# Kernel optimization log

Hardware: AMD Instinct MI355X
Metric: run time of the kernel (lower is better)

Reference implementation:

```python
import jax, jax.numpy as jnp
import numpy as np

T, B, D, H, L = 1024, 64, 512, 512, 2


def setup_inputs() -> dict:
    key = jax.random.key(0)
    ks = jax.random.split(key, 10)
    s = 1.0 / np.sqrt(D)
    return {
        "x": jax.random.normal(ks[0], (T, B, D), jnp.float32),
        "hidden": jax.random.normal(ks[1], (L, B, H), jnp.float32),
        "fc_w": jax.random.normal(ks[2], (D, D), jnp.float32) * s,
        "fc_b": jax.random.normal(ks[3], (D,), jnp.float32) * s,
        "w0": jax.random.normal(ks[4], (H, D), jnp.float32) * s,
        "b0": jax.random.normal(ks[5], (H,), jnp.float32) * s,
        "u0": jax.random.uniform(ks[6], (H,), jnp.float32, -1.0, 1.0),
        "w1": jax.random.normal(ks[7], (H, H), jnp.float32) * s,
        "b1": jax.random.normal(ks[8], (H,), jnp.float32) * s,
        "u1": jax.random.uniform(ks[9], (H,), jnp.float32, -1.0, 1.0),
    }


def _indrnn_layer(inp, h0, w, b, u):
    # Precompute input projection for all timesteps: [T, B, H]
    pre = jnp.einsum("tbd,hd->tbh", inp, w) + b

    def step(h, p):
        h_new = jax.nn.relu(p + u * h)  # elementwise recurrent weight
        return h_new, h_new

    h_last, outs = jax.lax.scan(step, h0, pre)
    return outs, h_last


def reference(x, hidden, fc_w, fc_b, w0, b0, u0, w1, b1, u1):
    # fc layer before the IndRNN stack
    x = jnp.einsum("tbd,ed->tbe", x, fc_w) + fc_b
    out0, h0 = _indrnn_layer(x, hidden[0], w0, b0, u0)
    out1, h1 = _indrnn_layer(out0, hidden[1], w1, b1, u1)
    hn = jnp.stack([h0, h1], axis=0)  # [L, B, H]
    return out1, hn
```

## Files before the change

### kernel.cpp

```cpp
#include <hip/hip_runtime.h>
#include <hip/hip_bf16.h>
#include <cstdint>
#include <cstddef>

#define T_DIM 1024
#define B_DIM 64
#define D_DIM 512
#define H_DIM 512
#define TBROWS (T_DIM * B_DIM)
#define BH (B_DIM * H_DIM)
#define TBH ((size_t)T_DIM * (size_t)BH)

typedef __bf16 bf16x8 __attribute__((ext_vector_type(8)));
typedef float floatx4 __attribute__((ext_vector_type(4)));

__device__ __forceinline__ void async_load16(const void* g, void* l) {
  __builtin_amdgcn_global_load_lds(
      (const __attribute__((address_space(1))) unsigned int*)g,
      (__attribute__((address_space(3))) unsigned int*)l,
      16, 0, 0);
}

__global__ __launch_bounds__(256) void cvt_bf16_kernel(
    const float* __restrict__ in, __bf16* __restrict__ out, long n) {
  long i = ((long)blockIdx.x * 256 + threadIdx.x) * 8;
  if (i + 8 <= n) {
    const float4 a = *(const float4*)(in + i);
    const float4 b = *(const float4*)(in + i + 4);
    bf16x8 v;
    v[0] = (__bf16)a.x; v[1] = (__bf16)a.y; v[2] = (__bf16)a.z; v[3] = (__bf16)a.w;
    v[4] = (__bf16)b.x; v[5] = (__bf16)b.y; v[6] = (__bf16)b.z; v[7] = (__bf16)b.w;
    *(bf16x8*)(out + i) = v;
  }
}

__global__ __launch_bounds__(256) void prep_kernel(
    const float* __restrict__ w0, const float* __restrict__ fc_w,
    const float* __restrict__ fc_b, const float* __restrict__ b0,
    const float* __restrict__ w1, __bf16* __restrict__ Wc,
    __bf16* __restrict__ w1bf, float* __restrict__ bcomb) {
  const int blk = blockIdx.x;
  if (blk < 1024) {
    const int h = blk >> 1;
    const int d = ((blk & 1) << 8) + threadIdx.x;
    float a0 = 0.f, a1 = 0.f, a2 = 0.f, a3 = 0.f;
    for (int e = 0; e < D_DIM; e += 4) {
      a0 = fmaf(w0[h * D_DIM + e + 0], fc_w[(size_t)(e + 0) * D_DIM + d], a0);
      a1 = fmaf(w0[h * D_DIM + e + 1], fc_w[(size_t)(e + 1) * D_DIM + d], a1);
      a2 = fmaf(w0[h * D_DIM + e + 2], fc_w[(size_t)(e + 2) * D_DIM + d], a2);
      a3 = fmaf(w0[h * D_DIM + e + 3], fc_w[(size_t)(e + 3) * D_DIM + d], a3);
    }
    Wc[(size_t)h * D_DIM + d] = (__bf16)((a0 + a1) + (a2 + a3));
  } else if (blk < 1152) {
    const long i = ((long)(blk - 1024) * 256 + threadIdx.x) * 8;
    const float4 a = *(const float4*)(w1 + i);
    const float4 b = *(const float4*)(w1 + i + 4);
    bf16x8 v;
    v[0] = (__bf16)a.x; v[1] = (__bf16)a.y; v[2] = (__bf16)a.z; v[3] = (__bf16)a.w;
    v[4] = (__bf16)b.x; v[5] = (__bf16)b.y; v[6] = (__bf16)b.z; v[7] = (__bf16)b.w;
    *(bf16x8*)(w1bf + i) = v;
  } else {
    const int h = (blk - 1152) * 256 + threadIdx.x;
    float acc = b0[h];
    for (int e = 0; e < D_DIM; ++e)
      acc = fmaf(w0[(size_t)h * D_DIM + e], fc_b[e], acc);
    bcomb[h] = acc;
  }
}

#define BM 128
#define BN 128
#define BK 32

__global__ __launch_bounds__(256) void gemm_bt_bias(
    const __bf16* __restrict__ A,
    const __bf16* __restrict__ Bm,
    const float* __restrict__ bias,
    __bf16* __restrict__ C,
    int M, int N, int K) {
  __shared__ __bf16 As[BM * BK];
  __shared__ __bf16 Bs[BN * BK];

  const int tid = threadIdx.x;
  const int lane = tid & 63;
  const int wave = tid >> 6;
  const int nb = N / BN;
  const int bm = blockIdx.x / nb;
  const int bn = blockIdx.x % nb;
  const int m0 = bm * BM, n0 = bn * BN;

  floatx4 zero = {0.f, 0.f, 0.f, 0.f};
  floatx4 acc[4][4];
#pragma unroll
  for (int i = 0; i < 4; i++)
#pragma unroll
    for (int j = 0; j < 4; j++) acc[i][j] = zero;

  const int e0 = (wave * 2 + 0) * 64 + lane;
  const int e1 = (wave * 2 + 1) * 64 + lane;
  const int r0 = e0 >> 2, c0 = (e0 & 3) * 8;
  const int r1 = e1 >> 2, c1 = (e1 & 3) * 8;

  const int tm = (wave >> 1) * 64;
  const int tn = (wave & 1) * 64;
  const int lrow = lane & 15;
  const int lk = (lane >> 4) * 8;

  for (int k0 = 0; k0 < K; k0 += BK) {
    async_load16(&A[(size_t)(m0 + r0) * K + k0 + c0], &As[(wave * 2 + 0) * 512]);
    async_load16(&A[(size_t)(m0 + r1) * K + k0 + c1], &As[(wave * 2 + 1) * 512]);
    async_load16(&Bm[(size_t)(n0 + r0) * K + k0 + c0], &Bs[(wave * 2 + 0) * 512]);
    async_load16(&Bm[(size_t)(n0 + r1) * K + k0 + c1], &Bs[(wave * 2 + 1) * 512]);
    __syncthreads();

    bf16x8 af[4], bfr[4];
#pragma unroll
    for (int i = 0; i < 4; i++) {
      af[i]  = *(const bf16x8*)&As[(tm + i * 16 + lrow) * BK + lk];
      bfr[i] = *(const bf16x8*)&Bs[(tn + i * 16 + lrow) * BK + lk];
    }
#pragma unroll
    for (int i = 0; i < 4; i++)
#pragma unroll
      for (int j = 0; j < 4; j++)
        acc[i][j] = __builtin_amdgcn_mfma_f32_16x16x32_bf16(af[i], bfr[j],
                                                            acc[i][j], 0, 0, 0);
    __syncthreads();
  }

  const int ccol = lane & 15;
  const int crow = (lane >> 4) * 4;
  float bv[4];
#pragma unroll
  for (int j = 0; j < 4; j++) bv[j] = bias[n0 + tn + j * 16 + ccol];
#pragma unroll
  for (int i = 0; i < 4; i++) {
#pragma unroll
    for (int j = 0; j < 4; j++) {
      const size_t base =
          (size_t)(m0 + tm + i * 16 + crow) * N + (n0 + tn + j * 16 + ccol);
#pragma unroll
      for (int r = 0; r < 4; r++)
        C[base + (size_t)r * N] = (__bf16)(acc[i][j][r] + bv[j]);
    }
  }
}

#define TS 64
template <bool BF16OUT>
__global__ __launch_bounds__(64, 1) void scan_kernel(
    const __bf16* __restrict__ pre,
    const float* __restrict__ h0,
    const float* __restrict__ u,
    void* __restrict__ outp,
    float* __restrict__ hn) {
  __shared__ __bf16 tin[2][TS * 64];

  const int lane = threadIdx.x;
  const int c0 = blockIdx.x * 64;
  const int idx = c0 + lane;
  const float uu = u[idx & (H_DIM - 1)];
  float h = h0[idx];
  __bf16* __restrict__ ob = (__bf16*)outp;
  float* __restrict__ of = (float*)outp;

  const int lrow = lane >> 3;
  const int lcg = (lane & 7) * 8;

#pragma unroll
  for (int i = 0; i < 8; i++)
    async_load16(&pre[(size_t)(i * 8 + lrow) * BH + c0 + lcg], &tin[0][i * 512]);

  const int NT = T_DIM / TS;
  for (int tile = 0; tile < NT; tile++) {
    const int buf = tile & 1;
    const int t0 = tile * TS;
    if (tile + 1 < NT) {
      const int nt0 = (tile + 1) * TS;
#pragma unroll
      for (int i = 0; i < 8; i++)
        async_load16(&pre[(size_t)(nt0 + i * 8 + lrow) * BH + c0 + lcg],
                     &tin[buf ^ 1][i * 512]);
    }
    __syncthreads();
#pragma unroll
    for (int s = 0; s < TS; s++) {
      const float p = (float)tin[buf][s * 64 + lane];
      h = fmaxf(fmaf(uu, h, p), 0.0f);
      if (BF16OUT)
        ob[(size_t)(t0 + s) * BH + idx] = (__bf16)h;
      else
        of[(size_t)(t0 + s) * BH + idx] = h;
    }
    __syncthreads();
  }
  hn[idx] = h;
}

extern "C" void kernel_launch(void* const* d_in, const int* in_sizes, int n_in,
                              void* d_out, int out_size, void* d_ws,
                              size_t ws_size, hipStream_t stream) {
  (void)in_sizes; (void)n_in; (void)out_size; (void)ws_size;
  const float* x      = (const float*)d_in[0];
  const float* hidden = (const float*)d_in[1];
  const float* fc_w   = (const float*)d_in[2];
  const float* fc_b   = (const float*)d_in[3];
  const float* w0     = (const float*)d_in[4];
  const float* b0     = (const float*)d_in[5];
  const float* u0     = (const float*)d_in[6];
  const float* w1     = (const float*)d_in[7];
  const float* b1     = (const float*)d_in[8];
  const float* u1     = (const float*)d_in[9];
  float* out = (float*)d_out;

  char* ws = (char*)d_ws;
  __bf16* xbf  = (__bf16*)ws;
  __bf16* pre  = (__bf16*)(ws + TBH * 2);
  __bf16* out0 = (__bf16*)(ws + 2 * TBH * 2);
  char*   tail = ws + 3 * TBH * 2;
  __bf16* Wc    = (__bf16*)tail;
  __bf16* w1bf  = (__bf16*)(tail + 512 * 1024);
  float*  bcomb = (float*)(tail + 1024 * 1024);

  float* hn = out + TBH;

  prep_kernel<<<1154, 256, 0, stream>>>(w0, fc_w, fc_b, b0, w1, Wc, w1bf, bcomb);
  cvt_bf16_kernel<<<(int)(TBH / (256 * 8)), 256, 0, stream>>>(x, xbf, (long)TBH);
  gemm_bt_bias<<<(TBROWS / BM) * (H_DIM / BN), 256, 0, stream>>>(
      xbf, Wc, bcomb, pre, TBROWS, H_DIM, D_DIM);
  scan_kernel<true><<<BH / 64, 64, 0, stream>>>(pre, hidden, u0, (void*)out0, hn);
  gemm_bt_bias<<<(TBROWS / BM) * (H_DIM / BN), 256, 0, stream>>>(
      out0, w1bf, b1, pre, TBROWS, H_DIM, H_DIM);
  scan_kernel<false><<<BH / 64, 64, 0, stream>>>(pre, hidden + BH, u1,
                                                 (void*)out, hn + BH);
}
```

Measured before the change: 451.6 us.

## Fuse x bf16 conversion into GEMM, deepen scan pipeline, swizzle XCDs, speed prep

The first GEMM now loads fp32 x directly into LDS with an XOR swizzle and converts it to bf16 while building fragments, so the separate conversion kernel and its intermediate buffer are gone. Both GEMMs remap block IDs so neighbouring tiles land on the same XCD. The scan kernel gains a third input buffer with explicit vmcnt waits in place of barriers. It also stages outputs in LDS so global stores become coalesced 16-byte writes. The prep kernel computes 8 rows per thread and reads the bias GEMV with vectorised loads, at the cost of more LDS and hand-tuned wait counts that must stay correct.

```diff
diff --git a/kernel.cpp b/kernel.cpp
--- a/kernel.cpp
+++ b/kernel.cpp
@@ -21,16 +21,14 @@
       16, 0, 0);
 }
 
-__global__ __launch_bounds__(256) void cvt_bf16_kernel(
-    const float* __restrict__ in, __bf16* __restrict__ out, long n) {
-  long i = ((long)blockIdx.x * 256 + threadIdx.x) * 8;
-  if (i + 8 <= n) {
-    const float4 a = *(const float4*)(in + i);
-    const float4 b = *(const float4*)(in + i + 4);
-    bf16x8 v;
-    v[0] = (__bf16)a.x; v[1] = (__bf16)a.y; v[2] = (__bf16)a.z; v[3] = (__bf16)a.w;
-    v[4] = (__bf16)b.x; v[5] = (__bf16)b.y; v[6] = (__bf16)b.z; v[7] = (__bf16)b.w;
-    *(bf16x8*)(out + i) = v;
+__device__ __forceinline__ void wait_vm(int n) {
+  switch (n) {
+    case 16: asm volatile("s_waitcnt vmcnt(16)" ::: "memory"); break;
+    case 24: asm volatile("s_waitcnt vmcnt(24)" ::: "memory"); break;
+    case 32: asm volatile("s_waitcnt vmcnt(32)" ::: "memory"); break;
+    case 40: asm volatile("s_waitcnt vmcnt(40)" ::: "memory"); break;
+    case 48: asm volatile("s_waitcnt vmcnt(48)" ::: "memory"); break;
+    default: asm volatile("s_waitcnt vmcnt(0)" ::: "memory"); break;
   }
 }
 
@@ -40,19 +38,25 @@
     const float* __restrict__ w1, __bf16* __restrict__ Wc,
     __bf16* __restrict__ w1bf, float* __restrict__ bcomb) {
   const int blk = blockIdx.x;
-  if (blk < 1024) {
-    const int h = blk >> 1;
-    const int d = ((blk & 1) << 8) + threadIdx.x;
-    float a0 = 0.f, a1 = 0.f, a2 = 0.f, a3 = 0.f;
-    for (int e = 0; e < D_DIM; e += 4) {
-      a0 = fmaf(w0[h * D_DIM + e + 0], fc_w[(size_t)(e + 0) * D_DIM + d], a0);
-      a1 = fmaf(w0[h * D_DIM + e + 1], fc_w[(size_t)(e + 1) * D_DIM + d], a1);
-      a2 = fmaf(w0[h * D_DIM + e + 2], fc_w[(size_t)(e + 2) * D_DIM + d], a2);
-      a3 = fmaf(w0[h * D_DIM + e + 3], fc_w[(size_t)(e + 3) * D_DIM + d], a3);
-    }
-    Wc[(size_t)h * D_DIM + d] = (__bf16)((a0 + a1) + (a2 + a3));
-  } else if (blk < 1152) {
-    const long i = ((long)(blk - 1024) * 256 + threadIdx.x) * 8;
+  const int tid = threadIdx.x;
+  if (blk < 128) {
+    const int h0 = (blk >> 1) * 8;
+    const int d = ((blk & 1) << 8) + tid;
+    float a[8];
+#pragma unroll
+    for (int j = 0; j < 8; j++) a[j] = 0.f;
+#pragma unroll 4
+    for (int e = 0; e < D_DIM; ++e) {
+      const float fv = fc_w[(size_t)e * D_DIM + d];
+#pragma unroll
+      for (int j = 0; j < 8; j++)
+        a[j] = fmaf(w0[(size_t)(h0 + j) * D_DIM + e], fv, a[j]);
+    }
+#pragma unroll
+    for (int j = 0; j < 8; j++)
+      Wc[(size_t)(h0 + j) * D_DIM + d] = (__bf16)a[j];
+  } else if (blk < 256) {
+    const long i = ((long)(blk - 128) * 256 + tid) * 8;
     const float4 a = *(const float4*)(w1 + i);
     const float4 b = *(const float4*)(w1 + i + 4);
     bf16x8 v;
@@ -60,10 +64,17 @@
     v[4] = (__bf16)b.x; v[5] = (__bf16)b.y; v[6] = (__bf16)b.z; v[7] = (__bf16)b.w;
     *(bf16x8*)(w1bf + i) = v;
   } else {
-    const int h = (blk - 1152) * 256 + threadIdx.x;
+    const int h = (blk - 256) * 256 + tid;
     float acc = b0[h];
-    for (int e = 0; e < D_DIM; ++e)
-      acc = fmaf(w0[(size_t)h * D_DIM + e], fc_b[e], acc);
+    const float4* w4 = (const float4*)(w0 + (size_t)h * D_DIM);
+#pragma unroll 4
+    for (int e = 0; e < D_DIM / 4; ++e) {
+      const float4 wv = w4[e];
+      acc = fmaf(wv.x, fc_b[e * 4 + 0], acc);
+      acc = fmaf(wv.y, fc_b[e * 4 + 1], acc);
+      acc = fmaf(wv.z, fc_b[e * 4 + 2], acc);
+      acc = fmaf(wv.w, fc_b[e * 4 + 3], acc);
+    }
     bcomb[h] = acc;
   }
 }
@@ -71,6 +82,100 @@
 #define BM 128
 #define BN 128
 #define BK 32
+
+__device__ __forceinline__ int xcd_swizzle(int bid, int nwg) {
+  return (bid & 7) * (nwg >> 3) + (bid >> 3);
+}
+
+__global__ __launch_bounds__(256) void gemm_a32_bt_bias(
+    const float* __restrict__ A,
+    const __bf16* __restrict__ Bm,
+    const float* __restrict__ bias,
+    __bf16* __restrict__ C,
+    int M, int N, int K) {
+  __shared__ float Asf[BM * BK];
+  __shared__ __bf16 Bs[BN * BK];
+
+  const int tid = threadIdx.x;
+  const int lane = tid & 63;
+  const int wave = tid >> 6;
+  const int wg = xcd_swizzle((int)blockIdx.x, (int)gridDim.x);
+  const int nb = N / BN;
+  const int bm = wg / nb;
+  const int bn = wg % nb;
+  const int m0 = bm * BM, n0 = bn * BN;
+
+  floatx4 zero = {0.f, 0.f, 0.f, 0.f};
+  floatx4 acc[4][4];
+#pragma unroll
+  for (int i = 0; i < 4; i++)
+#pragma unroll
+    for (int j = 0; j < 4; j++) acc[i][j] = zero;
+
+  const int e0 = (wave * 2 + 0) * 64 + lane;
+  const int e1 = (wave * 2 + 1) * 64 + lane;
+  const int r0 = e0 >> 2, c0 = (e0 & 3) * 8;
+  const int r1 = e1 >> 2, c1 = (e1 & 3) * 8;
+
+  const int tm = (wave >> 1) * 64;
+  const int tn = (wave & 1) * 64;
+  const int lrow = lane & 15;
+  const int lk = (lane >> 4) * 8;
+
+  const int ea = wave * 4;
+
+  for (int k0 = 0; k0 < K; k0 += BK) {
+#pragma unroll
+    for (int i = 0; i < 4; i++) {
+      const int e = (ea + i) * 64 + lane;
+      const int r = e >> 3;
+      const int sg = (e & 7) ^ (r & 7);
+      async_load16(&A[(size_t)(m0 + r) * K + k0 + sg * 4], &Asf[(ea + i) * 256]);
+    }
+    async_load16(&Bm[(size_t)(n0 + r0) * K + k0 + c0], &Bs[(wave * 2 + 0) * 512]);
+    async_load16(&Bm[(size_t)(n0 + r1) * K + k0 + c1], &Bs[(wave * 2 + 1) * 512]);
+    __syncthreads();
+
+    bf16x8 af[4], bfr[4];
+#pragma unroll
+    for (int i = 0; i < 4; i++) {
+      const int row = tm + i * 16 + lrow;
+      const int k7 = row & 7;
+      const int s0 = lk >> 2;
+      const float4 fa = *(const float4*)&Asf[row * BK + ((s0 ^ k7) << 2)];
+      const float4 fb = *(const float4*)&Asf[row * BK + (((s0 + 1) ^ k7) << 2)];
+      bf16x8 v;
+      v[0] = (__bf16)fa.x; v[1] = (__bf16)fa.y; v[2] = (__bf16)fa.z; v[3] = (__bf16)fa.w;
+      v[4] = (__bf16)fb.x; v[5] = (__bf16)fb.y; v[6] = (__bf16)fb.z; v[7] = (__bf16)fb.w;
+      af[i] = v;
+      bfr[i] = *(const bf16x8*)&Bs[(tn + i * 16 + lrow) * BK + lk];
+    }
+#pragma unroll
+    for (int i = 0; i < 4; i++)
+#pragma unroll
+      for (int j = 0; j < 4; j++)
+        acc[i][j] = __builtin_amdgcn_mfma_f32_16x16x32_bf16(af[i], bfr[j],
+                                                            acc[i][j], 0, 0, 0);
+    __syncthreads();
+  }
+
+  const int ccol = lane & 15;
+  const int crow = (lane >> 4) * 4;
+  float bv[4];
+#pragma unroll
+  for (int j = 0; j < 4; j++) bv[j] = bias[n0 + tn + j * 16 + ccol];
+#pragma unroll
+  for (int i = 0; i < 4; i++) {
+#pragma unroll
+    for (int j = 0; j < 4; j++) {
+      const size_t base =
+          (size_t)(m0 + tm + i * 16 + crow) * N + (n0 + tn + j * 16 + ccol);
+#pragma unroll
+      for (int r = 0; r < 4; r++)
+        C[base + (size_t)r * N] = (__bf16)(acc[i][j][r] + bv[j]);
+    }
+  }
+}
 
 __global__ __launch_bounds__(256) void gemm_bt_bias(
     const __bf16* __restrict__ A,
@@ -84,9 +189,10 @@
   const int tid = threadIdx.x;
   const int lane = tid & 63;
   const int wave = tid >> 6;
+  const int wg = xcd_swizzle((int)blockIdx.x, (int)gridDim.x);
   const int nb = N / BN;
-  const int bm = blockIdx.x / nb;
-  const int bn = blockIdx.x % nb;
+  const int bm = wg / nb;
+  const int bn = wg % nb;
   const int m0 = bm * BM, n0 = bn * BN;
 
   floatx4 zero = {0.f, 0.f, 0.f, 0.f};
@@ -147,6 +253,8 @@
 }
 
 #define TS 64
+#define NTILE (T_DIM / TS)
+
 template <bool BF16OUT>
 __global__ __launch_bounds__(64, 1) void scan_kernel(
     const __bf16* __restrict__ pre,
@@ -154,15 +262,15 @@
     const float* __restrict__ u,
     void* __restrict__ outp,
     float* __restrict__ hn) {
-  __shared__ __bf16 tin[2][TS * 64];
+  constexpr int OBYTES = BF16OUT ? 2 : 4;
+  __shared__ __bf16 tin[3][TS * 64];
+  __shared__ char oraw[2][TS * 64 * OBYTES];
 
   const int lane = threadIdx.x;
   const int c0 = blockIdx.x * 64;
   const int idx = c0 + lane;
   const float uu = u[idx & (H_DIM - 1)];
   float h = h0[idx];
-  __bf16* __restrict__ ob = (__bf16*)outp;
-  float* __restrict__ of = (float*)outp;
 
   const int lrow = lane >> 3;
   const int lcg = (lane & 7) * 8;
@@ -170,29 +278,59 @@
 #pragma unroll
   for (int i = 0; i < 8; i++)
     async_load16(&pre[(size_t)(i * 8 + lrow) * BH + c0 + lcg], &tin[0][i * 512]);
-
-  const int NT = T_DIM / TS;
-  for (int tile = 0; tile < NT; tile++) {
-    const int buf = tile & 1;
+#pragma unroll
+  for (int i = 0; i < 8; i++)
+    async_load16(&pre[(size_t)(TS + i * 8 + lrow) * BH + c0 + lcg],
+                 &tin[1][i * 512]);
+
+  for (int tile = 0; tile < NTILE; ++tile) {
+    __builtin_amdgcn_sched_barrier(0);
+    if (tile + 2 < NTILE) {
+      const int nb = (tile + 2) % 3;
+      const size_t nt0 = (size_t)(tile + 2) * TS;
+#pragma unroll
+      for (int i = 0; i < 8; i++)
+        async_load16(&pre[(nt0 + i * 8 + lrow) * BH + c0 + lcg],
+                     &tin[nb][i * 512]);
+    }
+    int wv;
+    if (BF16OUT)
+      wv = (tile == 0 || tile == NTILE - 1) ? 16
+         : (tile == 1 || tile == NTILE - 2) ? 24 : 32;
+    else
+      wv = (tile == 0) ? 16
+         : (tile == 1 || tile == NTILE - 1) ? 32
+         : (tile == NTILE - 2) ? 40 : 48;
+    wait_vm(wv);
+    __builtin_amdgcn_sched_barrier(0);
+
+    const int buf = tile % 3;
     const int t0 = tile * TS;
-    if (tile + 1 < NT) {
-      const int nt0 = (tile + 1) * TS;
-#pragma unroll
-      for (int i = 0; i < 8; i++)
-        async_load16(&pre[(size_t)(nt0 + i * 8 + lrow) * BH + c0 + lcg],
-                     &tin[buf ^ 1][i * 512]);
-    }
-    __syncthreads();
+    char* ob = oraw[tile & 1];
 #pragma unroll
     for (int s = 0; s < TS; s++) {
       const float p = (float)tin[buf][s * 64 + lane];
       h = fmaxf(fmaf(uu, h, p), 0.0f);
-      if (BF16OUT)
-        ob[(size_t)(t0 + s) * BH + idx] = (__bf16)h;
-      else
-        of[(size_t)(t0 + s) * BH + idx] = h;
-    }
-    __syncthreads();
+      if (BF16OUT) ((__bf16*)ob)[s * 64 + lane] = (__bf16)h;
+      else         ((float*)ob)[s * 64 + lane] = h;
+    }
+    if (BF16OUT) {
+#pragma unroll
+      for (int i = 0; i < 8; i++) {
+        const int row = i * 8 + (lane >> 3);
+        const bf16x8 v =
+            *(const bf16x8*)&((const __bf16*)ob)[row * 64 + (lane & 7) * 8];
+        *(bf16x8*)&((__bf16*)outp)[(size_t)(t0 + row) * BH + c0 + (lane & 7) * 8] = v;
+      }
+    } else {
+#pragma unroll
+      for (int i = 0; i < 16; i++) {
+        const int row = i * 4 + (lane >> 4);
+        const float4 v =
+            *(const float4*)&((const float*)ob)[row * 64 + (lane & 15) * 4];
+        *(float4*)&((float*)outp)[(size_t)(t0 + row) * BH + c0 + (lane & 15) * 4] = v;
+      }
+    }
   }
   hn[idx] = h;
 }
@@ -214,20 +352,18 @@
   float* out = (float*)d_out;
 
   char* ws = (char*)d_ws;
-  __bf16* xbf  = (__bf16*)ws;
-  __bf16* pre  = (__bf16*)(ws + TBH * 2);
-  __bf16* out0 = (__bf16*)(ws + 2 * TBH * 2);
-  char*   tail = ws + 3 * TBH * 2;
+  __bf16* pre  = (__bf16*)ws;
+  __bf16* out0 = (__bf16*)(ws + TBH * 2);
+  char*   tail = ws + 2 * TBH * 2;
   __bf16* Wc    = (__bf16*)tail;
   __bf16* w1bf  = (__bf16*)(tail + 512 * 1024);
   float*  bcomb = (float*)(tail + 1024 * 1024);
 
   float* hn = out + TBH;
 
-  prep_kernel<<<1154, 256, 0, stream>>>(w0, fc_w, fc_b, b0, w1, Wc, w1bf, bcomb);
-  cvt_bf16_kernel<<<(int)(TBH / (256 * 8)), 256, 0, stream>>>(x, xbf, (long)TBH);
-  gemm_bt_bias<<<(TBROWS / BM) * (H_DIM / BN), 256, 0, stream>>>(
-      xbf, Wc, bcomb, pre, TBROWS, H_DIM, D_DIM);
+  prep_kernel<<<258, 256, 0, stream>>>(w0, fc_w, fc_b, b0, w1, Wc, w1bf, bcomb);
+  gemm_a32_bt_bias<<<(TBROWS / BM) * (H_DIM / BN), 256, 0, stream>>>(
+      x, Wc, bcomb, pre, TBROWS, H_DIM, D_DIM);
   scan_kernel<true><<<BH / 64, 64, 0, stream>>>(pre, hidden, u0, (void*)out0, hn);
   gemm_bt_bias<<<(TBROWS / BM) * (H_DIM / BN), 256, 0, stream>>>(
       out0, w1bf, b1, pre, TBROWS, H_DIM, H_DIM);
```

Result: no change. 452.5 us (+0.2%).
